# Performance work log

Measured on AMD Instinct MI355X. Metric: run time of the kernel, lower is better.

## Reference

```python
import jax, jax.numpy as jnp
import numpy as np

# --- static configuration (mirrors PMETorchPME(alpha=1.0, mesh=1.0), interpolation_nodes=6) ---
ALPHA = 1.0            # Gaussian smearing sigma of CoulombPotential
MESH_SPACING = 1.0
BOX_L = 120.0
NS = (120, 120, 120)   # ceil(BOX_L / MESH_SPACING) per axis; static for jit
ORDER = 6              # interpolation nodes (6-point stencil per axis)
N_ATOMS = 100000
PI = np.pi


def _interp_weights(x):
    # x: (N,3) offsets in [-0.5, 0.5) relative to the midpoint of the 6-point stencil.
    # Lagrange interpolation on nodes t_j = j - 2.5, j = 0..5 (even-order, midpoint-centered).
    t = np.arange(ORDER) - (ORDER - 1) / 2.0                 # (6,) node positions
    diff = x[..., None] - jnp.asarray(t, x.dtype)            # (N,3,6)
    ws = []
    for j in range(ORDER):
        idx = [k for k in range(ORDER) if k != j]
        denom = float(np.prod([t[j] - t[k] for k in idx]))
        ws.append(jnp.prod(diff[..., idx], axis=-1) / denom)
    return jnp.stack(ws, axis=-1)                            # (N,3,6)


def _stencil(coords, box):
    # Map positions to mesh units, build per-particle 6x6x6 stencil weights + flat mesh indices.
    frac = coords @ jnp.linalg.inv(box)                      # fractional coordinates
    pos = frac * jnp.asarray(NS, coords.dtype)               # (N,3) in mesh units
    i0 = jnp.floor(pos)
    x = pos - (i0 + 0.5)                                     # offset from stencil midpoint
    w = _interp_weights(x)                                   # (N,3,6)
    offs = jnp.arange(ORDER, dtype=jnp.int32) - (ORDER // 2 - 1)   # [-2..3]
    ns_i = jnp.asarray(NS, jnp.int32)
    g = (i0.astype(jnp.int32)[..., None] + offs) % ns_i[None, :, None]  # (N,3,6) periodic
    W = w[:, 0, :, None, None] * w[:, 1, None, :, None] * w[:, 2, None, None, :]   # (N,6,6,6)
    flat = (g[:, 0, :, None, None] * NS[1] + g[:, 1, None, :, None]) * NS[2] + g[:, 2, None, None, :]
    n = coords.shape[0]
    return W.reshape(n, -1), flat.reshape(n, -1)             # (N,216) each


def _kspace_kernel(box, dtype):
    # G(k) = 4*pi * exp(-sigma^2 k^2 / 2) / k^2, zero at k=0 (CoulombPotential.lr_from_k_sq)
    inv_cell = jnp.linalg.inv(box)
    m0 = jnp.fft.fftfreq(NS[0]) * NS[0]
    m1 = jnp.fft.fftfreq(NS[1]) * NS[1]
    m2 = jnp.fft.rfftfreq(NS[2]) * NS[2]
    m = jnp.stack(jnp.meshgrid(m0, m1, m2, indexing="ij"), axis=-1).astype(dtype)
    k = 2.0 * PI * jnp.einsum("xyzm,nm->xyzn", m, inv_cell)  # k = 2*pi * inv(cell) @ m
    k_sq = jnp.sum(k * k, axis=-1)
    safe = jnp.where(k_sq > 0, k_sq, 1.0)
    return jnp.where(k_sq > 0, 4.0 * PI * jnp.exp(-0.5 * ALPHA * ALPHA * k_sq) / safe, 0.0)


def setup_inputs() -> dict:
    key = jax.random.key(0)
    k1, k2 = jax.random.split(key)
    coords = jax.random.uniform(k1, (N_ATOMS, 3), dtype=jnp.float32) * BOX_L
    box = (BOX_L * jnp.eye(3, dtype=jnp.float32))
    charges = jax.random.normal(k2, (N_ATOMS, 1), dtype=jnp.float32)
    return {"coords": coords, "box": box, "charges": charges}


def reference(coords, box, charges):
    q = charges[:, 0]                                        # (N,)
    W, flat = _stencil(coords, box)                          # (N,216)
    ntot = NS[0] * NS[1] * NS[2]
    # charge spreading (scatter-add)
    mesh = jnp.zeros((ntot,), coords.dtype).at[flat.reshape(-1)].add((W * q[:, None]).reshape(-1))
    mesh = mesh.reshape(NS)
    # FFT convolution with the reciprocal-space Coulomb kernel
    G = _kspace_kernel(box, coords.dtype)
    pot_mesh = jnp.fft.irfftn(jnp.fft.rfftn(mesh, norm="backward") * G, s=NS, norm="forward")
    # gather back to particles
    pot = jnp.sum(pot_mesh.reshape(-1)[flat] * W, axis=-1)   # (N,)
    volume = jnp.abs(jnp.linalg.det(box))
    pot = pot / volume
    pot = pot - q * (np.sqrt(2.0 / PI) / ALPHA)              # remove self-contribution
    pot = pot - 2.0 * (PI * ALPHA * ALPHA) * jnp.sum(q) / volume  # charge-neutral background
    pot = pot / 2.0
    return jnp.sum(q * pot)                                  # energy = sum(charges * potentials)
```

## Files before the change

kernel.cpp:

```cpp
#include <hip/hip_runtime.h>
#include <math.h>

#define NMESH 120
#define NKZ 61
#define ALPHA_C 1.0

#define TILE 12
#define NTPD 10
#define NTILE 1000
#define FP 17
#define ZPAD 20
#define FPSTRIDE 5792
#define CAP 256

#define CHUNK 128
#define WXA_OFF 0
#define WYA_OFF (CHUNK*ZPAD)
#define WZA_OFF (2*CHUNK*ZPAD)
#define LYS_OFF (3*CHUNK*ZPAD)
#define SMEMF   (LYS_OFF + CHUNK)

#define YCH 12
#define XCH 4
#define YROW 137

#define NSLOT 64
#define SLOTSTRIDE 8
#define W120C (-0.052359877559829887f)

typedef float v2f __attribute__((ext_vector_type(2)));

#define EK_OFF      0
#define Q_OFF       4096
#define Q2_OFF      8192
#define BUF_OFF     115264
#define C1_OFF      23283264
#define C2_OFF      115264
#define COUNTS_OFF  C1_OFF
#define SORTED_OFF  (C1_OFF + 4096)

__device__ inline void inv3(const float* b, float* ib) {
    float a00=b[0],a01=b[1],a02=b[2],a10=b[3],a11=b[4],a12=b[5],a20=b[6],a21=b[7],a22=b[8];
    float c00 =  a11*a22 - a12*a21;
    float c01 = -(a10*a22 - a12*a20);
    float c02 =  a10*a21 - a11*a20;
    float c10 = -(a01*a22 - a02*a21);
    float c11 =  a00*a22 - a02*a20;
    float c12 = -(a00*a21 - a01*a20);
    float c20 =  a01*a12 - a02*a11;
    float c21 = -(a00*a12 - a02*a10);
    float c22 =  a00*a11 - a01*a10;
    float det = a00*c00 + a01*c01 + a02*c02;
    float inv = 1.0f/det;
    ib[0]=c00*inv; ib[1]=c10*inv; ib[2]=c20*inv;
    ib[3]=c01*inv; ib[4]=c11*inv; ib[5]=c21*inv;
    ib[6]=c02*inv; ib[7]=c12*inv; ib[8]=c22*inv;
}

__device__ inline void atom_pos(const float* __restrict__ box, float c0, float c1, float c2,
                                float* p) {
    float ib[9]; inv3(box, ib);
    #pragma unroll
    for (int d=0; d<3; ++d)
        p[d] = (c0*ib[0+d] + c1*ib[3+d] + c2*ib[6+d]) * 120.0f;
}

__device__ inline int wrap120(int i) { return ((i % 120) + 120) % 120; }

__device__ inline void lag6(float x, float* w) {
    float df[6];
    #pragma unroll
    for (int k=0;k<6;++k) df[k] = x - ((float)k - 2.5f);
    w[0] = df[1]*df[2]*df[3]*df[4]*df[5] * (-1.0f/120.0f);
    w[1] = df[0]*df[2]*df[3]*df[4]*df[5] * ( 1.0f/24.0f);
    w[2] = df[0]*df[1]*df[3]*df[4]*df[5] * (-1.0f/12.0f);
    w[3] = df[0]*df[1]*df[2]*df[4]*df[5] * ( 1.0f/12.0f);
    w[4] = df[0]*df[1]*df[2]*df[3]*df[5] * (-1.0f/24.0f);
    w[5] = df[0]*df[1]*df[2]*df[3]*df[4] * ( 1.0f/120.0f);
}

__device__ inline int halo_pairs(int c, int* t, int* l) {
    int r = c % 12, ti = c / 12, n = 0;
    t[n] = ti;          l[n] = r + 2;  n++;
    if (r < 3)  { t[n] = (ti+9)%10; l[n] = r + 14; n++; }
    if (r >= 10){ t[n] = (ti+1)%10; l[n] = r - 10; n++; }
    return n;
}

__device__ inline void dft8(const float2* xin, float2* Y) {
    const float S = 0.70710678118654752f;
    float2 a=xin[0], b=xin[2], c=xin[4], d=xin[6];
    float s02r=a.x+c.x, s02i=a.y+c.y, d02r=a.x-c.x, d02i=a.y-c.y;
    float s13r=b.x+d.x, s13i=b.y+d.y, d13r=b.x-d.x, d13i=b.y-d.y;
    float2 E0 = make_float2(s02r+s13r, s02i+s13i);
    float2 E1 = make_float2(d02r+d13i, d02i-d13r);
    float2 E2 = make_float2(s02r-s13r, s02i-s13i);
    float2 E3 = make_float2(d02r-d13i, d02i+d13r);
    a=xin[1]; b=xin[3]; c=xin[5]; d=xin[7];
    s02r=a.x+c.x; s02i=a.y+c.y; d02r=a.x-c.x; d02i=a.y-c.y;
    s13r=b.x+d.x; s13i=b.y+d.y; d13r=b.x-d.x; d13i=b.y-d.y;
    float2 O0 = make_float2(s02r+s13r, s02i+s13i);
    float2 O1 = make_float2(d02r+d13i, d02i-d13r);
    float2 O2 = make_float2(s02r-s13r, s02i-s13i);
    float2 O3 = make_float2(d02r-d13i, d02i+d13r);
    float t1r = S*(O1.x + O1.y), t1i = S*(O1.y - O1.x);
    float t2r = O2.y,            t2i = -O2.x;
    float t3r = S*(O3.y - O3.x), t3i = -S*(O3.x + O3.y);
    Y[0] = make_float2(E0.x + O0.x, E0.y + O0.y);
    Y[4] = make_float2(E0.x - O0.x, E0.y - O0.y);
    Y[1] = make_float2(E1.x + t1r,  E1.y + t1i);
    Y[5] = make_float2(E1.x - t1r,  E1.y - t1i);
    Y[2] = make_float2(E2.x + t2r,  E2.y + t2i);
    Y[6] = make_float2(E2.x - t2r,  E2.y - t2i);
    Y[3] = make_float2(E3.x + t3r,  E3.y + t3i);
    Y[7] = make_float2(E3.x - t3r,  E3.y - t3i);
}

__global__ void scatter_q_kernel(const float* __restrict__ coords,
                                 const float* __restrict__ box,
                                 const float* __restrict__ charges,
                                 int* __restrict__ counts,
                                 float4* __restrict__ sorted,
                                 double* __restrict__ qslots,
                                 double* __restrict__ q2slots, int n) {
    int i = blockIdx.x*blockDim.x + threadIdx.x;
    float v = 0.f, v2 = 0.f;
    if (i < n) {
        float p[3]; atom_pos(box, coords[3*i], coords[3*i+1], coords[3*i+2], p);
        float q = charges[i];
        v = q; v2 = q*q;
        int t[3];
        #pragma unroll
        for (int d=0; d<3; ++d) t[d] = wrap120((int)floorf(p[d])) / TILE;
        int tile = (t[0]*NTPD + t[1])*NTPD + t[2];
        int idx = atomicAdd(&counts[tile], 1);
        if (idx < CAP) sorted[tile*CAP + idx] = make_float4(p[0], p[1], p[2], q);
    }
    #pragma unroll
    for (int o=32;o>0;o>>=1) { v += __shfl_down(v,o,64); v2 += __shfl_down(v2,o,64); }
    __shared__ float s1[4], s2[4];
    int lane = threadIdx.x & 63, w = threadIdx.x >> 6;
    if (lane==0) { s1[w]=v; s2[w]=v2; }
    __syncthreads();
    if (threadIdx.x==0) {
        for (int j=1;j<4;j++) { v += s1[j]; v2 += s2[j]; }
        int slot = (blockIdx.x & (NSLOT-1)) * SLOTSTRIDE;
        atomicAdd(&qslots[slot],  (double)v);
        atomicAdd(&q2slots[slot], (double)v2);
    }
}

__global__ void __launch_bounds__(128, 4)
spread_tile_kernel(const float4* __restrict__ sorted,
                   const int* __restrict__ counts,
                   float* __restrict__ buf) {
    int tile = blockIdx.x;
    int tx = tile / (NTPD*NTPD);
    int rem = tile - tx*NTPD*NTPD;
    int ty = rem / NTPD;
    int tz = rem - ty*NTPD;
    int bx = tx*TILE, by = ty*TILE, bz = tz*TILE;

    __shared__ float smem[SMEMF];
    int* lys = (int*)&smem[LYS_OFF];

    int tid = threadIdx.x;
    int b = tid / 17;
    int A = tid - b*17;
    int bc = (b > 4) ? 4 : b;
    bool owner = (tid < 85);

    v2f acc[34];
    #pragma unroll
    for (int i=0;i<34;++i) acc[i] = (v2f){0.f, 0.f};

    int cntT = min(counts[tile], CAP);
    const float4* src = sorted + (size_t)tile*CAP;

    for (int start = 0; start < cntT; start += CHUNK) {
        int jn = cntT - start; if (jn > CHUNK) jn = CHUNK;
        __syncthreads();
        if (tid < jn) {
            float4 s = src[start + tid];
            float fx = floorf(s.x), fy = floorf(s.y), fz = floorf(s.z);
            float wx[6]; lag6(s.x - (fx + 0.5f), wx);
            float wy[6]; lag6(s.y - (fy + 0.5f), wy);
            float wz[6]; lag6(s.z - (fz + 0.5f), wz);
            int lx = wrap120((int)fx) - bx;
            int ly = wrap120((int)fy) - by;
            int lz = wrap120((int)fz) - bz;
            float4 z4 = make_float4(0.f,0.f,0.f,0.f);
            float4* px = (float4*)&smem[WXA_OFF + tid*ZPAD];
            float4* py = (float4*)&smem[WYA_OFF + tid*ZPAD];
            float4* pz = (float4*)&smem[WZA_OFF + tid*ZPAD];
            #pragma unroll
            for (int k=0;k<5;++k) { px[k]=z4; py[k]=z4; pz[k]=z4; }
            #pragma unroll
            for (int k=0;k<6;++k) {
                smem[WXA_OFF + tid*ZPAD + lx + k] = wx[k];
                smem[WYA_OFF + tid*ZPAD + ly + k] = wy[k];
                smem[WZA_OFF + tid*ZPAD + lz + k] = wz[k]*s.w;
            }
            lys[tid] = ly;
        }
        __syncthreads();
        auto body = [&](int j) {
            float wx_ = smem[WXA_OFF + j*ZPAD + A];
            float4 wy4 = *(const float4*)&smem[WYA_OFF + j*ZPAD + 4*bc];
            const float4* zp = (const float4*)&smem[WZA_OFF + j*ZPAD];
            float4 z0 = zp[0], z1 = zp[1], z2 = zp[2], z3 = zp[3];
            float z16 = smem[WZA_OFF + j*ZPAD + 16];
            v2f w2a = (v2f){wx_*wy4.x, wx_*wy4.y};
            v2f w2b = (v2f){wx_*wy4.z, wx_*wy4.w};
            float zv[17];
            zv[0]=z0.x;  zv[1]=z0.y;  zv[2]=z0.z;  zv[3]=z0.w;
            zv[4]=z1.x;  zv[5]=z1.y;  zv[6]=z1.z;  zv[7]=z1.w;
            zv[8]=z2.x;  zv[9]=z2.y;  zv[10]=z2.z; zv[11]=z2.w;
            zv[12]=z3.x; zv[13]=z3.y; zv[14]=z3.z; zv[15]=z3.w;
            zv[16]=z16;
            #pragma unroll
            for (int k=0;k<17;++k) {
                v2f zz = (v2f){zv[k], zv[k]};
                acc[2*k]   += w2a * zz;
                acc[2*k+1] += w2b * zz;
            }
        };
        if (tid < 64) {
            #pragma unroll 2
            for (int j = 0; j < jn; ++j) body(j);
        } else {
            int lane = tid & 63;
            int l0 = lys[lane], l1 = lys[64 + lane];
            bool g0 = (lane < jn)      && (l0 >= 7);
            bool g1 = (64 + lane < jn) && (l1 >= 7);
            unsigned long long m0 = __ballot(g0);
            unsigned long long m1 = __ballot(g1);
            while (m0) { int j = __builtin_ctzll(m0); m0 &= m0-1ull; body(j); }
            while (m1) { int j = 64 + __builtin_ctzll(m1); m1 &= m1-1ull; body(j); }
        }
    }
    __syncthreads();
    if (owner) {
        #pragma unroll
        for (int db=0; db<4; ++db) {
            int Bv = 4*b + db;
            if (Bv <= 16) {
                float vals[17];
                #pragma unroll
                for (int k=0;k<17;++k)
                    vals[k] = (db & 1) ? acc[2*k + (db>>1)].y : acc[2*k + (db>>1)].x;
                float* dst = &smem[(A*17 + Bv)*ZPAD];
                *(float4*)&dst[0]  = make_float4(vals[0], vals[1], vals[2], vals[3]);
                *(float4*)&dst[4]  = make_float4(vals[4], vals[5], vals[6], vals[7]);
                *(float4*)&dst[8]  = make_float4(vals[8], vals[9], vals[10],vals[11]);
                *(float4*)&dst[12] = make_float4(vals[12],vals[13],vals[14],vals[15]);
                dst[16] = vals[16];
            }
        }
    }
    __syncthreads();
    float4* bp = (float4*)(buf + (size_t)tile * FPSTRIDE);
    const float4* sp = (const float4*)smem;
    for (int i = tid; i < FPSTRIDE/4; i += 128) bp[i] = sp[i];
}

#define DFT15_BODY(Yp, kfreq, RE, IM)                                        \
    float w1r = tw[kfreq].x, w1i = tw[kfreq].y;                              \
    float w2r = w1r*w1r - w1i*w1i, w2i = 2.f*w1r*w1i;                        \
    float w3r = w2r*w1r - w2i*w1i, w3i = w2r*w1i + w2i*w1r;                  \
    float ar=1.f, ai=0.f, br=w1r, bi=w1i, cr=w2r, ci=w2i;                    \
    float r0_=0.f,i0_=0.f,r1_=0.f,i1_=0.f,r2_=0.f,i2_=0.f;                   \
    _Pragma("unroll")                                                        \
    for (int s_=0;s_<5;++s_) {                                               \
        float2 ya = (Yp)[3*s_], yb = (Yp)[3*s_+1], yc = (Yp)[3*s_+2];        \
        r0_ = fmaf(ya.x, ar, fmaf(-ya.y, ai, r0_));                          \
        i0_ = fmaf(ya.x, ai, fmaf( ya.y, ar, i0_));                          \
        r1_ = fmaf(yb.x, br, fmaf(-yb.y, bi, r1_));                          \
        i1_ = fmaf(yb.x, bi, fmaf( yb.y, br, i1_));                          \
        r2_ = fmaf(yc.x, cr, fmaf(-yc.y, ci, r2_));                          \
        i2_ = fmaf(yc.x, ci, fmaf( yc.y, cr, i2_));                          \
        float n_;                                                            \
        n_ = ar*w3r - ai*w3i; ai = ar*w3i + ai*w3r; ar = n_;                 \
        n_ = br*w3r - bi*w3i; bi = br*w3i + bi*w3r; br = n_;                 \
        n_ = cr*w3r - ci*w3i; ci = cr*w3i + ci*w3r; cr = n_;                 \
    }                                                                        \
    float RE = (r0_+r1_)+r2_, IM = (i0_+i1_)+i2_;

#define TWIDDLE_INIT()                                                       \
    __shared__ float2 tw[120];                                               \
    for (int k_ = threadIdx.x; k_ < 120; k_ += blockDim.x) {                 \
        float s_, c_; __sincosf(W120C * (float)k_, &s_, &c_);                \
        tw[k_] = make_float2(c_, s_);                                        \
    }

__global__ void __launch_bounds__(256)
fft_z_kernel(const float* __restrict__ buf,
             float2* __restrict__ C1) {
    int x  = blockIdx.x / 10;
    int y0 = (blockIdx.x - x*10) * YCH;
    __shared__ float  lin[YCH][121];
    __shared__ float2 Ys[YCH][YROW];
    TWIDDLE_INIT()

    int txA[2], lxA[2];
    int nx = halo_pairs(x, txA, lxA);

    for (int i = threadIdx.x; i < YCH*120; i += 256) {
        int yl = i / 120, z = i - yl*120;
        int tyA[2], lyA[2]; int ny = halo_pairs(y0 + yl, tyA, lyA);
        int tzA[2], lzA[2]; int nz = halo_pairs(z, tzA, lzA);
        float s = 0.f;
        for (int ii=0; ii<nx; ++ii)
            for (int jj=0; jj<ny; ++jj)
                for (int kk=0; kk<nz; ++kk) {
                    int tile = (txA[ii]*NTPD + tyA[jj])*NTPD + tzA[kk];
                    int cell = (lxA[ii]*FP + lyA[jj])*ZPAD + lzA[kk];
                    s += buf[(size_t)tile*FPSTRIDE + cell];
                }
        lin[yl][z] = s;
    }
    __syncthreads();
    for (int t = threadIdx.x; t < YCH*15; t += 256) {
        int yl = t / 15, j = t - (t/15)*15;
        float2 xin[8], Yo[8];
        #pragma unroll
        for (int m=0;m<8;++m) xin[m] = make_float2(lin[yl][15*m+j], 0.f);
        dft8(xin, Yo);
        #pragma unroll
        for (int r=0;r<8;++r) Ys[yl][r*17+j] = Yo[r];
    }
    __syncthreads();
    for (int o = threadIdx.x; o < YCH*NKZ; o += 256) {
        int kz = o / YCH, yl = o - (o/YCH)*YCH;
        const float2* Yp = &Ys[yl][(kz&7)*17];
        DFT15_BODY(Yp, kz, re, im)
        C1[(x*NKZ + kz)*120 + y0 + yl] = make_float2(re, im);
    }
}

__global__ void __launch_bounds__(256)
fft_y_kernel(const float2* __restrict__ C1,
             float2* __restrict__ C2) {
    int xc = blockIdx.x / NKZ;
    int kz = blockIdx.x - xc*NKZ;
    int x0 = xc * XCH;
    __shared__ float2 lin[XCH][121];
    __shared__ float2 Ys[XCH][YROW];
    TWIDDLE_INIT()
    for (int i = threadIdx.x; i < XCH*120; i += 256) {
        int xo = i / 120, y = i - (i/120)*120;
        lin[xo][y] = C1[((x0+xo)*NKZ + kz)*120 + y];
    }
    __syncthreads();
    for (int t = threadIdx.x; t < XCH*15; t += 256) {
        int xo = t / 15, j = t - (t/15)*15;
        float2 xin[8], Yo[8];
        #pragma unroll
        for (int m=0;m<8;++m) xin[m] = lin[xo][15*m+j];
        dft8(xin, Yo);
        #pragma unroll
        for (int r=0;r<8;++r) Ys[xo][r*17+j] = Yo[r];
    }
    __syncthreads();
    for (int o = threadIdx.x; o < XCH*120; o += 256) {
        int ky = o >> 2, xo = o & 3;
        const float2* Yp = &Ys[xo][(ky&7)*17];
        DFT15_BODY(Yp, ky, re, im)
        C2[(kz*120 + ky)*120 + x0 + xo] = make_float2(re, im);
    }
}

__global__ void __launch_bounds__(256)
fft_x_energy_kernel(const float2* __restrict__ C2,
                    const float* __restrict__ box,
                    double* __restrict__ ekslots) {
    int kyc = blockIdx.x / NKZ;
    int kz  = blockIdx.x - kyc*NKZ;
    int ky0 = kyc * XCH;
    __shared__ float2 lin[XCH][121];
    __shared__ float2 Ys[XCH][YROW];
    TWIDDLE_INIT()
    const float2* src = C2 + (kz*120 + ky0)*120;
    for (int i = threadIdx.x; i < XCH*120; i += 256) {
        int kyo = i / 120, xx = i - (i/120)*120;
        lin[kyo][xx] = src[i];
    }
    __syncthreads();
    for (int t = threadIdx.x; t < XCH*15; t += 256) {
        int kyo = t / 15, j = t - (t/15)*15;
        float2 xin[8], Yo[8];
        #pragma unroll
        for (int m=0;m<8;++m) xin[m] = lin[kyo][15*m+j];
        dft8(xin, Yo);
        #pragma unroll
        for (int r=0;r<8;++r) Ys[kyo][r*17+j] = Yo[r];
    }
    __syncthreads();
    float ib[9]; inv3(box, ib);
    const float TWOPI = 6.283185307179586f;
    float wzf = (kz==0 || kz==60) ? 1.0f : 2.0f;
    float contrib = 0.f;
    for (int o = threadIdx.x; o < XCH*120; o += 256) {
        int kyo = o / 120, kx = o - (o/120)*120;
        int ky = ky0 + kyo;
        const float2* Yp = &Ys[kyo][(kx&7)*17];
        DFT15_BODY(Yp, kx, re, im)
        if (!(kx==0 && ky==0 && kz==0)) {
            float mx = (kx < 60) ? (float)kx : (float)(kx - 120);
            float my = (ky < 60) ? (float)ky : (float)(ky - 120);
            float mz = (float)kz;
            float k0 = TWOPI*(mx*ib[0] + my*ib[1] + mz*ib[2]);
            float k1 = TWOPI*(mx*ib[3] + my*ib[4] + mz*ib[5]);
            float k2 = TWOPI*(mx*ib[6] + my*ib[7] + mz*ib[8]);
            float ksq = k0*k0 + k1*k1 + k2*k2;
            float G = 12.566370614359172f * __expf(-0.5f*(float)(ALPHA_C*ALPHA_C)*ksq) / ksq;
            contrib += wzf * G * (re*re + im*im);
        }
    }
    #pragma unroll
    for (int o=32;o>0;o>>=1) contrib += __shfl_down(contrib,o,64);
    __shared__ float sm[4];
    int lane = threadIdx.x & 63, w = threadIdx.x >> 6;
    if (lane==0) sm[w] = contrib;
    __syncthreads();
    if (threadIdx.x==0)
        atomicAdd(&ekslots[(blockIdx.x & (NSLOT-1)) * SLOTSTRIDE],
                  (double)(sm[0]+sm[1]+sm[2]+sm[3]));
}

__global__ void finalize_kernel(const double* __restrict__ ekslots,
                                const double* __restrict__ qslots,
                                const double* __restrict__ q2slots,
                                const float* __restrict__ box,
                                float* __restrict__ out) {
    int lane = threadIdx.x;
    double ek  = ekslots[lane*SLOTSTRIDE];
    double sq  = qslots [lane*SLOTSTRIDE];
    double sq2 = q2slots[lane*SLOTSTRIDE];
    #pragma unroll
    for (int o=32;o>0;o>>=1) {
        ek  += __shfl_down(ek,  o, 64);
        sq  += __shfl_down(sq,  o, 64);
        sq2 += __shfl_down(sq2, o, 64);
    }
    if (lane == 0) {
        double a00=box[0],a01=box[1],a02=box[2],a10=box[3],a11=box[4],a12=box[5],a20=box[6],a21=box[7],a22=box[8];
        double det = a00*(a11*a22-a12*a21) - a01*(a10*a22-a12*a20) + a02*(a10*a21-a11*a20);
        double vol = fabs(det);
        double E = ek/(2.0*vol)
                 - 0.5*sqrt(2.0/M_PI)/ALPHA_C * sq2
                 - M_PI*ALPHA_C*ALPHA_C * sq*sq / vol;
        out[0] = (float)E;
    }
}

extern "C" void kernel_launch(void* const* d_in, const int* in_sizes, int n_in,
                              void* d_out, int out_size, void* d_ws, size_t ws_size,
                              hipStream_t stream) {
    const float* coords  = (const float*)d_in[0];
    const float* box     = (const float*)d_in[1];
    const float* charges = (const float*)d_in[2];
    int n = in_sizes[0] / 3;

    char* ws = (char*)d_ws;
    double* ekslots = (double*)(ws + EK_OFF);
    double* qslots  = (double*)(ws + Q_OFF);
    double* q2slots = (double*)(ws + Q2_OFF);
    float*  buf     = (float*) (ws + BUF_OFF);
    float2* C1      = (float2*)(ws + C1_OFF);
    float2* C2      = (float2*)(ws + C2_OFF);
    int* counts     = (int*)(ws + COUNTS_OFF);
    float4* sorted  = (float4*)(ws + SORTED_OFF);

    int gA = (n + 255)/256;
    hipMemsetAsync(ws + EK_OFF, 0, 3*4096, stream);
    hipMemsetAsync(ws + COUNTS_OFF, 0, NTILE*sizeof(int), stream);
    scatter_q_kernel<<<gA, 256, 0, stream>>>(coords, box, charges, counts, sorted, qslots, q2slots, n);
    spread_tile_kernel<<<NTILE, 128, 0, stream>>>(sorted, counts, buf);
    fft_z_kernel<<<120*10, 256, 0, stream>>>(buf, C1);
    fft_y_kernel<<<30*NKZ, 256, 0, stream>>>(C1, C2);
    fft_x_energy_kernel<<<NKZ*30, 256, 0, stream>>>(C2, box, ekslots);
    finalize_kernel<<<1, 64, 0, stream>>>(ekslots, qslots, q2slots, box, (float*)d_out);
}
```

Measured before the change: 153.2 us.

## Split spread-tile accumulation across four waves with y-range culling and two-half reduction

Raises the spread kernel to 256 threads (four waves). Each wave owns a 3-column slice of the 17x17x17 tile footprint and half of the particle chunk, and skips particles whose y-stencil cannot touch its y-range. The two particle halves are combined through shared memory in two serialized passes. The x/y weight arrays are repacked to stride 17. The goal is better load balance and less per-thread register pressure than the old scheme, where one wave walked every particle. The cost is extra synchronisation, a read-modify-write reduction pass, and some idle lanes (only 51 of 64 per wave own output).

```diff
diff --git a/kernel.cpp b/kernel.cpp
--- a/kernel.cpp
+++ b/kernel.cpp
@@ -15,9 +15,9 @@
 
 #define CHUNK 128
 #define WXA_OFF 0
-#define WYA_OFF (CHUNK*ZPAD)
-#define WZA_OFF (2*CHUNK*ZPAD)
-#define LYS_OFF (3*CHUNK*ZPAD)
+#define WYA_OFF (CHUNK*17)
+#define WZA_OFF (2*CHUNK*17)
+#define LYS_OFF (2*CHUNK*17 + CHUNK*20)
 #define SMEMF   (LYS_OFF + CHUNK)
 
 #define YCH 12
@@ -150,7 +150,7 @@
     }
 }
 
-__global__ void __launch_bounds__(128, 4)
+__global__ void __launch_bounds__(256, 4)
 spread_tile_kernel(const float4* __restrict__ sorted,
                    const int* __restrict__ counts,
                    float* __restrict__ buf) {
@@ -164,15 +164,25 @@
     __shared__ float smem[SMEMF];
     int* lys = (int*)&smem[LYS_OFF];
 
-    int tid = threadIdx.x;
-    int b = tid / 17;
-    int A = tid - b*17;
-    int bc = (b > 4) ? 4 : b;
-    bool owner = (tid < 85);
-
-    v2f acc[34];
+    int tid  = threadIdx.x;
+    int wv   = tid >> 6;
+    int lane = tid & 63;
+    int half = wv & 1;
+    int blo  = (wv < 2) ? 0 : 9;
+    int t3   = lane / 17; if (t3 > 2) t3 = 2;
+    int A    = lane - 17*t3; if (A > 16) A = 16;
+    bool owner = (lane < 51);
+    int B0   = blo + 3*t3;
+    bool c2ok = (B0 + 2 <= 16);
+
+    v2f   acc2[3][8];
+    float acc16[3];
     #pragma unroll
-    for (int i=0;i<34;++i) acc[i] = (v2f){0.f, 0.f};
+    for (int c=0;c<3;++c) {
+        #pragma unroll
+        for (int k=0;k<8;++k) acc2[c][k] = (v2f){0.f,0.f};
+        acc16[c] = 0.f;
+    }
 
     int cntT = min(counts[tile], CAP);
     const float4* src = sorted + (size_t)tile*CAP;
@@ -189,79 +199,91 @@
             int lx = wrap120((int)fx) - bx;
             int ly = wrap120((int)fy) - by;
             int lz = wrap120((int)fz) - bz;
+            #pragma unroll
+            for (int k=0;k<17;++k) { smem[WXA_OFF + tid*17 + k] = 0.f;
+                                     smem[WYA_OFF + tid*17 + k] = 0.f; }
             float4 z4 = make_float4(0.f,0.f,0.f,0.f);
-            float4* px = (float4*)&smem[WXA_OFF + tid*ZPAD];
-            float4* py = (float4*)&smem[WYA_OFF + tid*ZPAD];
             float4* pz = (float4*)&smem[WZA_OFF + tid*ZPAD];
             #pragma unroll
-            for (int k=0;k<5;++k) { px[k]=z4; py[k]=z4; pz[k]=z4; }
+            for (int k=0;k<5;++k) pz[k] = z4;
             #pragma unroll
             for (int k=0;k<6;++k) {
-                smem[WXA_OFF + tid*ZPAD + lx + k] = wx[k];
-                smem[WYA_OFF + tid*ZPAD + ly + k] = wy[k];
+                smem[WXA_OFF + tid*17 + lx + k] = wx[k];
+                smem[WYA_OFF + tid*17 + ly + k] = wy[k];
                 smem[WZA_OFF + tid*ZPAD + lz + k] = wz[k]*s.w;
             }
             lys[tid] = ly;
         }
         __syncthreads();
-        auto body = [&](int j) {
-            float wx_ = smem[WXA_OFF + j*ZPAD + A];
-            float4 wy4 = *(const float4*)&smem[WYA_OFF + j*ZPAD + 4*bc];
+        int j0  = half * 64;
+        int idx = j0 + lane;
+        int lyv = lys[idx];
+        bool g = (idx < jn) && (blo ? (lyv >= 4) : (lyv <= 8));
+        unsigned long long m = __ballot(g);
+        while (m) {
+            int j = j0 + __builtin_ctzll(m); m &= m - 1ull;
+            float wx_ = smem[WXA_OFF + j*17 + A];
+            float wy0 = smem[WYA_OFF + j*17 + B0];
+            float wy1 = smem[WYA_OFF + j*17 + B0 + 1];
+            float wy2 = smem[WYA_OFF + j*17 + B0 + 2];
+            float w2c[3];
+            w2c[0] = wx_*wy0;
+            w2c[1] = wx_*wy1;
+            w2c[2] = c2ok ? wx_*wy2 : 0.f;
             const float4* zp = (const float4*)&smem[WZA_OFF + j*ZPAD];
             float4 z0 = zp[0], z1 = zp[1], z2 = zp[2], z3 = zp[3];
             float z16 = smem[WZA_OFF + j*ZPAD + 16];
-            v2f w2a = (v2f){wx_*wy4.x, wx_*wy4.y};
-            v2f w2b = (v2f){wx_*wy4.z, wx_*wy4.w};
-            float zv[17];
-            zv[0]=z0.x;  zv[1]=z0.y;  zv[2]=z0.z;  zv[3]=z0.w;
-            zv[4]=z1.x;  zv[5]=z1.y;  zv[6]=z1.z;  zv[7]=z1.w;
-            zv[8]=z2.x;  zv[9]=z2.y;  zv[10]=z2.z; zv[11]=z2.w;
-            zv[12]=z3.x; zv[13]=z3.y; zv[14]=z3.z; zv[15]=z3.w;
-            zv[16]=z16;
+            v2f zz[8];
+            zz[0]=(v2f){z0.x,z0.y}; zz[1]=(v2f){z0.z,z0.w};
+            zz[2]=(v2f){z1.x,z1.y}; zz[3]=(v2f){z1.z,z1.w};
+            zz[4]=(v2f){z2.x,z2.y}; zz[5]=(v2f){z2.z,z2.w};
+            zz[6]=(v2f){z3.x,z3.y}; zz[7]=(v2f){z3.z,z3.w};
             #pragma unroll
-            for (int k=0;k<17;++k) {
-                v2f zz = (v2f){zv[k], zv[k]};
-                acc[2*k]   += w2a * zz;
-                acc[2*k+1] += w2b * zz;
-            }
-        };
-        if (tid < 64) {
-            #pragma unroll 2
-            for (int j = 0; j < jn; ++j) body(j);
-        } else {
-            int lane = tid & 63;
-            int l0 = lys[lane], l1 = lys[64 + lane];
-            bool g0 = (lane < jn)      && (l0 >= 7);
-            bool g1 = (64 + lane < jn) && (l1 >= 7);
-            unsigned long long m0 = __ballot(g0);
-            unsigned long long m1 = __ballot(g1);
-            while (m0) { int j = __builtin_ctzll(m0); m0 &= m0-1ull; body(j); }
-            while (m1) { int j = 64 + __builtin_ctzll(m1); m1 &= m1-1ull; body(j); }
-        }
-    }
-    __syncthreads();
-    if (owner) {
-        #pragma unroll
-        for (int db=0; db<4; ++db) {
-            int Bv = 4*b + db;
-            if (Bv <= 16) {
-                float vals[17];
+            for (int c=0;c<3;++c) {
+                v2f wv2 = (v2f){w2c[c], w2c[c]};
                 #pragma unroll
-                for (int k=0;k<17;++k)
-                    vals[k] = (db & 1) ? acc[2*k + (db>>1)].y : acc[2*k + (db>>1)].x;
-                float* dst = &smem[(A*17 + Bv)*ZPAD];
-                *(float4*)&dst[0]  = make_float4(vals[0], vals[1], vals[2], vals[3]);
-                *(float4*)&dst[4]  = make_float4(vals[4], vals[5], vals[6], vals[7]);
-                *(float4*)&dst[8]  = make_float4(vals[8], vals[9], vals[10],vals[11]);
-                *(float4*)&dst[12] = make_float4(vals[12],vals[13],vals[14],vals[15]);
-                dst[16] = vals[16];
+                for (int k=0;k<8;++k) acc2[c][k] += wv2 * zz[k];
+                acc16[c] = fmaf(w2c[c], z16, acc16[c]);
             }
         }
     }
     __syncthreads();
+    if ((half == 0) && owner) {
+        #pragma unroll
+        for (int c=0;c<3;++c) {
+            int Bc = B0 + c;
+            if (Bc <= 16) {
+                float* dst = &smem[(A*17 + Bc)*ZPAD];
+                *(float4*)&dst[0]  = make_float4(acc2[c][0].x, acc2[c][0].y, acc2[c][1].x, acc2[c][1].y);
+                *(float4*)&dst[4]  = make_float4(acc2[c][2].x, acc2[c][2].y, acc2[c][3].x, acc2[c][3].y);
+                *(float4*)&dst[8]  = make_float4(acc2[c][4].x, acc2[c][4].y, acc2[c][5].x, acc2[c][5].y);
+                *(float4*)&dst[12] = make_float4(acc2[c][6].x, acc2[c][6].y, acc2[c][7].x, acc2[c][7].y);
+                dst[16] = acc16[c];
+            }
+        }
+    }
+    __syncthreads();
+    if ((half == 1) && owner) {
+        #pragma unroll
+        for (int c=0;c<3;++c) {
+            int Bc = B0 + c;
+            if (Bc <= 16) {
+                float* dst = &smem[(A*17 + Bc)*ZPAD];
+                float4 a0 = *(float4*)&dst[0],  a1 = *(float4*)&dst[4];
+                float4 a2 = *(float4*)&dst[8],  a3 = *(float4*)&dst[12];
+                float  a4 = dst[16];
+                *(float4*)&dst[0]  = make_float4(a0.x+acc2[c][0].x, a0.y+acc2[c][0].y, a0.z+acc2[c][1].x, a0.w+acc2[c][1].y);
+                *(float4*)&dst[4]  = make_float4(a1.x+acc2[c][2].x, a1.y+acc2[c][2].y, a1.z+acc2[c][3].x, a1.w+acc2[c][3].y);
+                *(float4*)&dst[8]  = make_float4(a2.x+acc2[c][4].x, a2.y+acc2[c][4].y, a2.z+acc2[c][5].x, a2.w+acc2[c][5].y);
+                *(float4*)&dst[12] = make_float4(a3.x+acc2[c][6].x, a3.y+acc2[c][6].y, a3.z+acc2[c][7].x, a3.w+acc2[c][7].y);
+                dst[16] = a4 + acc16[c];
+            }
+        }
+    }
+    __syncthreads();
     float4* bp = (float4*)(buf + (size_t)tile * FPSTRIDE);
     const float4* sp = (const float4*)smem;
-    for (int i = tid; i < FPSTRIDE/4; i += 128) bp[i] = sp[i];
+    for (int i = tid; i < FPSTRIDE/4; i += 256) bp[i] = sp[i];
 }
 
 #define DFT15_BODY(Yp, kfreq, RE, IM)                                        \
@@ -476,7 +498,7 @@
     hipMemsetAsync(ws + EK_OFF, 0, 3*4096, stream);
     hipMemsetAsync(ws + COUNTS_OFF, 0, NTILE*sizeof(int), stream);
     scatter_q_kernel<<<gA, 256, 0, stream>>>(coords, box, charges, counts, sorted, qslots, q2slots, n);
-    spread_tile_kernel<<<NTILE, 128, 0, stream>>>(sorted, counts, buf);
+    spread_tile_kernel<<<NTILE, 256, 0, stream>>>(sorted, counts, buf);
     fft_z_kernel<<<120*10, 256, 0, stream>>>(buf, C1);
     fft_y_kernel<<<30*NKZ, 256, 0, stream>>>(C1, C2);
     fft_x_energy_kernel<<<NKZ*30, 256, 0, stream>>>(C2, box, ekslots);
```

Measured after the change: 150.1 us. 2.0% less time.
